# Kernel optimization log

Measured on AMD Instinct MI355X. Metric: run time of the kernel, lower is better.

The kernel has to match this reference:

```python
import jax, jax.numpy as jnp
import numpy as np

# Model dims (match init_kwargs)
E, D, H, K = 8, 512, 1024, 2   # num_experts, input/output dim, hidden dim, top_k
B, S = 4, 2048                 # batch, seq_len


def setup_inputs() -> dict:
    key = jax.random.key(0)
    ks = jax.random.split(key, 5)
    sd = lambda fan: np.float32(1.0 / np.sqrt(fan))
    return {
        "x": jax.random.normal(ks[0], (B, S, D), jnp.float32),
        "gate_w": jax.random.normal(ks[1], (D, E), jnp.float32) * sd(D),
        "gate_b": jnp.zeros((E,), jnp.float32),
        "w1": jax.random.normal(ks[2], (E, D, H), jnp.float32) * sd(D),
        "b1": jnp.zeros((E, H), jnp.float32),
        "w2": jax.random.normal(ks[3], (E, H, D), jnp.float32) * sd(H),
        "b2": jnp.zeros((E, D), jnp.float32),
    }


def reference(x, gate_w, gate_b, w1, b1, w2, b2):
    # x: [B, S, D]
    Bb, Ss, Dd = x.shape
    xf = x.reshape(-1, Dd)                              # [N, D], N = B*S

    # Router: softmax over experts, top-k, renormalize selected weights
    logits = xf @ gate_w + gate_b                        # [N, E]
    probs = jax.nn.softmax(logits, axis=-1)              # [N, E]
    top_w, top_i = jax.lax.top_k(probs, K)               # [N, K]
    top_w = top_w / top_w.sum(axis=-1, keepdims=True)

    # Per-token combine weight for each expert (0 if not routed).
    onehot = jax.nn.one_hot(top_i, E, dtype=probs.dtype)  # [N, K, E]
    combine = jnp.einsum("nke,nk->ne", onehot, top_w)     # [N, E]

    # Expert MLPs. Dropout is inactive at inference (identity).
    # h: [E, N, H]; GELU exact (torch nn.GELU default uses erf)
    h = jax.nn.gelu(jnp.einsum("nd,edh->enh", xf, w1) + b1[:, None, :],
                    approximate=False)
    y = jnp.einsum("enh,ehd->end", h, w2) + b2[:, None, :]  # [E, N, D]

    # Weighted combine: tokens not routed to expert e have combine[:, e] == 0.
    out = jnp.einsum("end,ne->nd", y, combine).reshape(Bb, Ss, Dd)
    return out, probs.reshape(Bb, Ss, E)
```

## Files before the change

kernel.cpp:

```cpp
#include <hip/hip_runtime.h>
#include <stdint.h>

#define N_TOK 8192
#define DIM   512
#define HID   1024
#define NE    8
#define NSLOT 16384
#define MAXSLOT 17408

typedef __attribute__((ext_vector_type(8))) short short8;
typedef __attribute__((ext_vector_type(4))) float f32x4;

#define W1T_OFF  0ull
#define W2T_OFF  8388608ull
#define H_OFF    16777216ull
#define Y_OFF    52428800ull
#define XBF_OFF  52428800ull
#define TOPI_OFF 70254592ull
#define TOPW_OFF 70320128ull
#define SLOT_OFF 70385664ull
#define ROWS_OFF 70451200ull
#define RW_OFF   70520832ull
#define CNT_OFF  70590464ull

__device__ __forceinline__ unsigned int f2bfu(float f) {
  union { float f; unsigned int i; } v; v.f = f;
  unsigned int u = v.i;
  return (u + 0x7FFFu + ((u >> 16) & 1u)) >> 16;
}
__device__ __forceinline__ float bf2f(unsigned int u) {
  union { unsigned int i; float f; } v; v.i = (u & 0xFFFFu) << 16; return v.f;
}
__device__ __forceinline__ float gelu_f(float x) {
  float x2 = x * x;
  float u = x * (1.59576912f + 0.07135481f * x2);
  float ez = __expf(-u);
  return x * __builtin_amdgcn_rcpf(1.0f + ez);
}
__device__ __forceinline__ void async16(void* lds, const void* g) {
  __builtin_amdgcn_global_load_lds(
      (const __attribute__((address_space(1))) unsigned int*)g,
      (__attribute__((address_space(3))) unsigned int*)lds, 16, 0, 0);
}

__global__ __launch_bounds__(256) void k_prep(
    const float* __restrict__ w1, const float* __restrict__ w2,
    unsigned short* __restrict__ w1t, unsigned short* __restrict__ w2t,
    const float* __restrict__ x, const float* __restrict__ gw,
    const float* __restrict__ gb, float* __restrict__ probs_out,
    int2* __restrict__ topi, float2* __restrict__ topw,
    unsigned short* __restrict__ xbf) {
  __shared__ unsigned short tile[64][68];
  int tid = threadIdx.x;
  if (blockIdx.x < 2048) {
    int b = blockIdx.x;
    const float* src; unsigned short* dst; int R, C;
    if (b < 1024) { int e = b >> 7; int t = b & 127;
      src = w1 + (size_t)e * 524288; dst = w1t + (size_t)e * 524288; R = 512; C = 1024;
      int tr = t >> 4, tc = t & 15;
      src += (size_t)tr * 64 * C + tc * 64; dst += (size_t)tc * 64 * R + tr * 64;
    } else { b -= 1024; int e = b >> 7; int t = b & 127;
      src = w2 + (size_t)e * 524288; dst = w2t + (size_t)e * 524288; R = 1024; C = 512;
      int tr = t >> 3, tc = t & 7;
      src += (size_t)tr * 64 * C + tc * 64; dst += (size_t)tc * 64 * R + tr * 64;
    }
#pragma unroll
    for (int i = 0; i < 4; ++i) {
      int l = i * 256 + tid;
      int r = l >> 4, c4 = (l & 15) << 2;
      float4 v = *(const float4*)(src + (size_t)r * C + c4);
      tile[r][c4 + 0] = (unsigned short)f2bfu(v.x);
      tile[r][c4 + 1] = (unsigned short)f2bfu(v.y);
      tile[r][c4 + 2] = (unsigned short)f2bfu(v.z);
      tile[r][c4 + 3] = (unsigned short)f2bfu(v.w);
    }
    __syncthreads();
#pragma unroll
    for (int i = 0; i < 2; ++i) {
      int l = i * 256 + tid;
      int rr = l >> 3, c8 = (l & 7) << 3;
      ushort4 a, b2v;
      a.x = tile[c8 + 0][rr]; a.y = tile[c8 + 1][rr];
      a.z = tile[c8 + 2][rr]; a.w = tile[c8 + 3][rr];
      b2v.x = tile[c8 + 4][rr]; b2v.y = tile[c8 + 5][rr];
      b2v.z = tile[c8 + 6][rr]; b2v.w = tile[c8 + 7][rr];
      uint4 pk;
      pk.x = (unsigned int)a.x | ((unsigned int)a.y << 16);
      pk.y = (unsigned int)a.z | ((unsigned int)a.w << 16);
      pk.z = (unsigned int)b2v.x | ((unsigned int)b2v.y << 16);
      pk.w = (unsigned int)b2v.z | ((unsigned int)b2v.w << 16);
      *(uint4*)(dst + (size_t)rr * R + c8) = pk;
    }
  } else {
    int wave = tid >> 6, lane = tid & 63;
    int n = (blockIdx.x - 2048) * 4 + wave;
    const float4* xr = (const float4*)(x + (size_t)n * DIM);
    float4 x0 = xr[lane * 2], x1 = xr[lane * 2 + 1];
    float xf[8] = {x0.x, x0.y, x0.z, x0.w, x1.x, x1.y, x1.z, x1.w};
    uint4 pa;
    pa.x = f2bfu(xf[0]) | (f2bfu(xf[1]) << 16);
    pa.y = f2bfu(xf[2]) | (f2bfu(xf[3]) << 16);
    pa.z = f2bfu(xf[4]) | (f2bfu(xf[5]) << 16);
    pa.w = f2bfu(xf[6]) | (f2bfu(xf[7]) << 16);
    *(uint4*)(xbf + (size_t)n * DIM + lane * 8) = pa;
    float acc[8] = {0.f,0.f,0.f,0.f,0.f,0.f,0.f,0.f};
    const float4* gwr = (const float4*)gw;
#pragma unroll
    for (int j = 0; j < 8; ++j) {
      int d = lane * 8 + j;
      float4 g0 = gwr[d * 2], g1 = gwr[d * 2 + 1];
      acc[0] += xf[j] * g0.x; acc[1] += xf[j] * g0.y; acc[2] += xf[j] * g0.z; acc[3] += xf[j] * g0.w;
      acc[4] += xf[j] * g1.x; acc[5] += xf[j] * g1.y; acc[6] += xf[j] * g1.z; acc[7] += xf[j] * g1.w;
    }
#pragma unroll
    for (int o = 1; o < 64; o <<= 1)
#pragma unroll
      for (int e = 0; e < 8; ++e) acc[e] += __shfl_xor(acc[e], o, 64);
    float p[8], mx = -1e30f, s = 0.f;
#pragma unroll
    for (int e = 0; e < 8; ++e) { p[e] = acc[e] + gb[e]; mx = fmaxf(mx, p[e]); }
#pragma unroll
    for (int e = 0; e < 8; ++e) { p[e] = __expf(p[e] - mx); s += p[e]; }
    float inv = 1.f / s;
#pragma unroll
    for (int e = 0; e < 8; ++e) p[e] *= inv;
    if (lane < 8) probs_out[(size_t)n * NE + lane] = p[lane];
    if (lane == 0) {
      int i0 = 0; float v0 = p[0];
#pragma unroll
      for (int e = 1; e < 8; ++e) if (p[e] > v0) { v0 = p[e]; i0 = e; }
      int i1 = -1; float v1 = -1.f;
#pragma unroll
      for (int e = 0; e < 8; ++e) if (e != i0 && p[e] > v1) { v1 = p[e]; i1 = e; }
      float sw = 1.f / (v0 + v1);
      topi[n] = make_int2(i0, i1);
      topw[n] = make_float2(v0 * sw, v1 * sw);
    }
  }
}

__global__ __launch_bounds__(1024) void k_countassign(
    const int2* __restrict__ topi, const float2* __restrict__ topw,
    int* __restrict__ meta, int* __restrict__ rows, float* __restrict__ rw,
    int* __restrict__ slot_of) {
  __shared__ int ch[32][8];
  __shared__ int tot[8], poff_s[9], tiles_s[8];
  __shared__ int sm_off[1024 * 8];
  int t = threadIdx.x, g = t >> 5;
  if (t < 256) ((int*)ch)[t] = 0;
  __syncthreads();
  int2 te[8]; float2 tw[8];
  int c[8] = {0,0,0,0,0,0,0,0};
  int base_tok = t * 8;
#pragma unroll
  for (int i = 0; i < 8; ++i) {
    te[i] = topi[base_tok + i];
    tw[i] = topw[base_tok + i];
#pragma unroll
    for (int k = 0; k < 8; ++k) c[k] += (te[i].x == k) + (te[i].y == k);
  }
#pragma unroll
  for (int k = 0; k < 8; ++k) if (c[k]) atomicAdd(&ch[g][k], c[k]);
#pragma unroll
  for (int k = 0; k < 8; ++k) {
    int s = c[k];
#pragma unroll
    for (int d = 1; d < 32; d <<= 1) {
      int u = __shfl_up(s, d, 32);
      if ((t & 31) >= d) s += u;
    }
    sm_off[t * 8 + k] = s - c[k];
  }
  __syncthreads();
  if (t < 8) {
    int a = 0;
#pragma unroll
    for (int b = 0; b < 32; ++b) { int v = ch[b][t]; ch[b][t] = a; a += v; }
    tot[t] = a; meta[t] = a;
  }
  __syncthreads();
  if (t == 0) {
    int a = 0, ts = 0;
#pragma unroll
    for (int e = 0; e < 8; ++e) {
      int tiles = (tot[e] + 127) >> 7;
      poff_s[e] = a; tiles_s[e] = tiles;
      meta[16 + e] = a; meta[32 + e] = ts;
      a += tiles << 7; ts += tiles;
    }
    poff_s[8] = a; meta[24] = a; meta[40] = ts;
  }
  __syncthreads();
#pragma unroll
  for (int i = 0; i < 8; ++i) {
    int n = base_tok + i;
    int e0 = te[i].x, e1 = te[i].y;
    int o0 = sm_off[t * 8 + e0]++;
    int s0 = poff_s[e0] + ch[g][e0] + o0;
    int o1 = sm_off[t * 8 + e1]++;
    int s1 = poff_s[e1] + ch[g][e1] + o1;
    rows[s0] = n; rw[s0] = tw[i].x; slot_of[2 * n] = s0;
    rows[s1] = n; rw[s1] = tw[i].y; slot_of[2 * n + 1] = s1;
  }
#pragma unroll
  for (int e = 0; e < 8; ++e) {
    int padn = (tiles_s[e] << 7) - tot[e];
    if (t < padn) {
      int s = poff_s[e] + tot[e] + t;
      rows[s] = 0; rw[s] = 0.f;
    }
  }
}

__global__ __launch_bounds__(256) void k_gemm1(
    const unsigned short* __restrict__ xbf, const unsigned short* __restrict__ w1t,
    const float* __restrict__ b1, const int* __restrict__ meta,
    const int* __restrict__ rows, unsigned short* __restrict__ h) {
  int lin = blockIdx.x;
  int xcd = lin & 7, j = lin >> 3;
  int t = xcd * 17 + (j >> 3);
  int nt = j & 7;
  if (t >= meta[40]) return;
  int e = 0;
#pragma unroll
  for (int i = 1; i < 8; ++i) if (t >= meta[32 + i]) e = i;
  int mt = t - meta[32 + e];
  int row0 = meta[16 + e] + (mt << 7);
  __shared__ __align__(16) unsigned short As[2][4096];
  __shared__ __align__(16) unsigned short Bs[2][4096];
  int tid = threadIdx.x;
  int wave = tid >> 6, lane = tid & 63;
  int wr = wave & 1, wc = wave >> 1;
  f32x4 acc[4][4] = {};
  const unsigned short* bBase = w1t + (size_t)e * HID * DIM + (size_t)(nt * 128) * DIM;

  const unsigned short* ga[2]; const unsigned short* gb[2];
#pragma unroll
  for (int jj = 0; jj < 2; ++jj) {
    int s = jj * 256 + tid;
    int r = s >> 2;
    int cg = ((s & 3) ^ ((r >> 1) & 3)) << 3;
    ga[jj] = xbf + (size_t)rows[row0 + r] * DIM + cg;
    gb[jj] = bBase + (size_t)r * DIM + cg;
  }
  int ldst = (wave * 64) * 8;

#pragma unroll
  for (int jj = 0; jj < 2; ++jj) {
    async16(&As[0][jj * 2048 + ldst], ga[jj]);
    async16(&Bs[0][jj * 2048 + ldst], gb[jj]);
  }
  __syncthreads();

  for (int k0 = 0; k0 < DIM; k0 += 32) {
    int cur = (k0 >> 5) & 1, nxt = cur ^ 1;
    if (k0 + 32 < DIM) {
#pragma unroll
      for (int jj = 0; jj < 2; ++jj) {
        async16(&As[nxt][jj * 2048 + ldst], ga[jj] + k0 + 32);
        async16(&Bs[nxt][jj * 2048 + ldst], gb[jj] + k0 + 32);
      }
    }
    {
      int ca = lane >> 4;
      short8 tf[4], wf[4];
#pragma unroll
      for (int am = 0; am < 4; ++am) {
        int ra = wr * 64 + am * 16 + (lane & 15);
        tf[am] = *(const short8*)&As[cur][(ra * 4 + (ca ^ ((ra >> 1) & 3))) * 8];
      }
#pragma unroll
      for (int an = 0; an < 4; ++an) {
        int rb = wc * 64 + an * 16 + (lane & 15);
        wf[an] = *(const short8*)&Bs[cur][(rb * 4 + (ca ^ ((rb >> 1) & 3))) * 8];
      }
#pragma unroll
      for (int an = 0; an < 4; ++an)
#pragma unroll
        for (int am = 0; am < 4; ++am)
          acc[an][am] = __builtin_amdgcn_mfma_f32_16x16x32_bf16(wf[an], tf[am], acc[an][am], 0, 0, 0);
    }
    __syncthreads();
  }
  int ml = lane & 15, q = lane >> 4;
#pragma unroll
  for (int am = 0; am < 4; ++am) {
    int slot_r = row0 + wr * 64 + am * 16 + ml;
    unsigned short* hrow = h + (size_t)slot_r * HID;
#pragma unroll
    for (int an = 0; an < 4; ++an) {
      int colb = nt * 128 + wc * 64 + an * 16 + q * 4;
      float4 bias = *(const float4*)&b1[e * HID + colb];
      f32x4 v = acc[an][am];
      float g0 = gelu_f(v[0] + bias.x);
      float g1 = gelu_f(v[1] + bias.y);
      float g2 = gelu_f(v[2] + bias.z);
      float g3 = gelu_f(v[3] + bias.w);
      uint2 pk;
      pk.x = f2bfu(g0) | (f2bfu(g1) << 16);
      pk.y = f2bfu(g2) | (f2bfu(g3) << 16);
      *(uint2*)(hrow + colb) = pk;
    }
  }
}

__global__ __launch_bounds__(256) void k_gemm2(
    const unsigned short* __restrict__ h, const unsigned short* __restrict__ w2t,
    const float* __restrict__ b2, const int* __restrict__ meta,
    const float* __restrict__ rw, unsigned short* __restrict__ y) {
  int lin = blockIdx.x;
  int xcd = lin & 7, j = lin >> 3;
  int t = xcd * 17 + (j >> 2);
  int nt = j & 3;
  if (t >= meta[40]) return;
  int e = 0;
#pragma unroll
  for (int i = 1; i < 8; ++i) if (t >= meta[32 + i]) e = i;
  int mt = t - meta[32 + e];
  int row0 = meta[16 + e] + (mt << 7);
  __shared__ __align__(16) unsigned short As[2][4096];
  __shared__ __align__(16) unsigned short Bs[2][4096];
  int tid = threadIdx.x;
  int wave = tid >> 6, lane = tid & 63;
  int wr = wave & 1, wc = wave >> 1;
  f32x4 acc[4][4] = {};
  const unsigned short* aBase = h + (size_t)row0 * HID;
  const unsigned short* bBase = w2t + (size_t)e * DIM * HID + (size_t)(nt * 128) * HID;

  const unsigned short* ga[2]; const unsigned short* gb[2];
#pragma unroll
  for (int jj = 0; jj < 2; ++jj) {
    int s = jj * 256 + tid;
    int r = s >> 2;
    int cg = ((s & 3) ^ ((r >> 1) & 3)) << 3;
    ga[jj] = aBase + (size_t)r * HID + cg;
    gb[jj] = bBase + (size_t)r * HID + cg;
  }
  int ldst = (wave * 64) * 8;

#pragma unroll
  for (int jj = 0; jj < 2; ++jj) {
    async16(&As[0][jj * 2048 + ldst], ga[jj]);
    async16(&Bs[0][jj * 2048 + ldst], gb[jj]);
  }
  __syncthreads();

  for (int k0 = 0; k0 < HID; k0 += 32) {
    int cur = (k0 >> 5) & 1, nxt = cur ^ 1;
    if (k0 + 32 < HID) {
#pragma unroll
      for (int jj = 0; jj < 2; ++jj) {
        async16(&As[nxt][jj * 2048 + ldst], ga[jj] + k0 + 32);
        async16(&Bs[nxt][jj * 2048 + ldst], gb[jj] + k0 + 32);
      }
    }
    {
      int ca = lane >> 4;
      short8 tf[4], wf[4];
#pragma unroll
      for (int am = 0; am < 4; ++am) {
        int ra = wr * 64 + am * 16 + (lane & 15);
        tf[am] = *(const short8*)&As[cur][(ra * 4 + (ca ^ ((ra >> 1) & 3))) * 8];
      }
#pragma unroll
      for (int an = 0; an < 4; ++an) {
        int rb = wc * 64 + an * 16 + (lane & 15);
        wf[an] = *(const short8*)&Bs[cur][(rb * 4 + (ca ^ ((rb >> 1) & 3))) * 8];
      }
#pragma unroll
      for (int an = 0; an < 4; ++an)
#pragma unroll
        for (int am = 0; am < 4; ++am)
          acc[an][am] = __builtin_amdgcn_mfma_f32_16x16x32_bf16(wf[an], tf[am], acc[an][am], 0, 0, 0);
    }
    __syncthreads();
  }
  int ml = lane & 15, q = lane >> 4;
#pragma unroll
  for (int am = 0; am < 4; ++am) {
    int slot_r = row0 + wr * 64 + am * 16 + ml;
    float w = rw[slot_r];
    unsigned short* yrow = y + (size_t)slot_r * DIM;
#pragma unroll
    for (int an = 0; an < 4; ++an) {
      int colb = nt * 128 + wc * 64 + an * 16 + q * 4;
      float4 bias = *(const float4*)&b2[e * DIM + colb];
      f32x4 v = acc[an][am];
      uint2 pk;
      pk.x = f2bfu((v[0] + bias.x) * w) | (f2bfu((v[1] + bias.y) * w) << 16);
      pk.y = f2bfu((v[2] + bias.z) * w) | (f2bfu((v[3] + bias.w) * w) << 16);
      *(uint2*)(yrow + colb) = pk;
    }
  }
}

__global__ __launch_bounds__(256) void k_combine(
    const unsigned short* __restrict__ y, const int* __restrict__ slot_of,
    float* __restrict__ out) {
  int t = blockIdx.x * 256 + threadIdx.x;
  int n = t >> 6, c = (t & 63) << 3;
  int s0 = slot_of[2 * n], s1 = slot_of[2 * n + 1];
  uint4 u0 = *(const uint4*)(y + (size_t)s0 * DIM + c);
  uint4 u1 = *(const uint4*)(y + (size_t)s1 * DIM + c);
  float4 o0, o1;
  o0.x = bf2f(u0.x) + bf2f(u1.x); o0.y = bf2f(u0.x >> 16) + bf2f(u1.x >> 16);
  o0.z = bf2f(u0.y) + bf2f(u1.y); o0.w = bf2f(u0.y >> 16) + bf2f(u1.y >> 16);
  o1.x = bf2f(u0.z) + bf2f(u1.z); o1.y = bf2f(u0.z >> 16) + bf2f(u1.z >> 16);
  o1.z = bf2f(u0.w) + bf2f(u1.w); o1.w = bf2f(u0.w >> 16) + bf2f(u1.w >> 16);
  *(float4*)(out + (size_t)n * DIM + c) = o0;
  *(float4*)(out + (size_t)n * DIM + c + 4) = o1;
}

extern "C" void kernel_launch(void* const* d_in, const int* in_sizes, int n_in,
                              void* d_out, int out_size, void* d_ws, size_t ws_size,
                              hipStream_t stream) {
  const float* x  = (const float*)d_in[0];
  const float* gw = (const float*)d_in[1];
  const float* gb = (const float*)d_in[2];
  const float* w1 = (const float*)d_in[3];
  const float* b1 = (const float*)d_in[4];
  const float* w2 = (const float*)d_in[5];
  const float* b2 = (const float*)d_in[6];
  float* out = (float*)d_out;
  char* ws = (char*)d_ws;

  unsigned short* w1t = (unsigned short*)(ws + W1T_OFF);
  unsigned short* w2t = (unsigned short*)(ws + W2T_OFF);
  unsigned short* h   = (unsigned short*)(ws + H_OFF);
  unsigned short* y   = (unsigned short*)(ws + Y_OFF);
  unsigned short* xbf = (unsigned short*)(ws + XBF_OFF);
  int2*   topi    = (int2*)(ws + TOPI_OFF);
  float2* topw    = (float2*)(ws + TOPW_OFF);
  int*    slot_of = (int*)(ws + SLOT_OFF);
  int*    rows    = (int*)(ws + ROWS_OFF);
  float*  rw      = (float*)(ws + RW_OFF);
  int*    meta    = (int*)(ws + CNT_OFF);
  float*  probs   = out + (size_t)N_TOK * DIM;

  k_prep       <<<dim3(4096), dim3(256),  0, stream>>>(w1, w2, w1t, w2t,
                                                       x, gw, gb, probs, topi, topw, xbf);
  k_countassign<<<dim3(1),    dim3(1024), 0, stream>>>(topi, topw, meta, rows, rw, slot_of);
  k_gemm1      <<<dim3(1088), dim3(256),  0, stream>>>(xbf, w1t, b1, meta, rows, h);
  k_gemm2      <<<dim3(544),  dim3(256),  0, stream>>>(h, w2t, b2, meta, rw, y);
  k_combine    <<<dim3(2048), dim3(256),  0, stream>>>(y, slot_of, out);
}
```

Baseline: 207.2 us.

## Load expert weight fragments directly from global, stage only activations in larger LDS chunks

Both expert GEMM kernels stop staging the weight (B) tile in shared memory. Each lane now reads its MFMA weight fragments straight from global memory. The activation (A) tile is staged in bigger 128-wide K chunks, double-buffered across 64 KB of LDS, so there are fewer barriers per K loop. This removes the LDS traffic and barriers for weights but makes MFMA issue wait on global/L2 latency for uncoalesced per-lane 16-byte weight loads. The larger LDS footprint may also reduce occupancy.

```diff
diff --git a/kernel.cpp b/kernel.cpp
--- a/kernel.cpp
+++ b/kernel.cpp
@@ -226,54 +226,52 @@
   for (int i = 1; i < 8; ++i) if (t >= meta[32 + i]) e = i;
   int mt = t - meta[32 + e];
   int row0 = meta[16 + e] + (mt << 7);
-  __shared__ __align__(16) unsigned short As[2][4096];
-  __shared__ __align__(16) unsigned short Bs[2][4096];
+  __shared__ __align__(16) unsigned short As[2][16384];
   int tid = threadIdx.x;
   int wave = tid >> 6, lane = tid & 63;
   int wr = wave & 1, wc = wave >> 1;
+  int ml = lane & 15, q = lane >> 4;
   f32x4 acc[4][4] = {};
   const unsigned short* bBase = w1t + (size_t)e * HID * DIM + (size_t)(nt * 128) * DIM;
 
-  const unsigned short* ga[2]; const unsigned short* gb[2];
-#pragma unroll
-  for (int jj = 0; jj < 2; ++jj) {
+  const unsigned short* wB[4];
+#pragma unroll
+  for (int an = 0; an < 4; ++an)
+    wB[an] = bBase + (size_t)(wc * 64 + an * 16 + ml) * DIM + q * 8;
+
+  const unsigned short* ga[8];
+#pragma unroll
+  for (int jj = 0; jj < 8; ++jj) {
     int s = jj * 256 + tid;
-    int r = s >> 2;
-    int cg = ((s & 3) ^ ((r >> 1) & 3)) << 3;
-    ga[jj] = xbf + (size_t)rows[row0 + r] * DIM + cg;
-    gb[jj] = bBase + (size_t)r * DIM + cg;
-  }
-  int ldst = (wave * 64) * 8;
-
-#pragma unroll
-  for (int jj = 0; jj < 2; ++jj) {
-    async16(&As[0][jj * 2048 + ldst], ga[jj]);
-    async16(&Bs[0][jj * 2048 + ldst], gb[jj]);
-  }
-  __syncthreads();
-
-  for (int k0 = 0; k0 < DIM; k0 += 32) {
-    int cur = (k0 >> 5) & 1, nxt = cur ^ 1;
-    if (k0 + 32 < DIM) {
-#pragma unroll
-      for (int jj = 0; jj < 2; ++jj) {
-        async16(&As[nxt][jj * 2048 + ldst], ga[jj] + k0 + 32);
-        async16(&Bs[nxt][jj * 2048 + ldst], gb[jj] + k0 + 32);
+    int ks = s >> 9, r = (s >> 2) & 127, c2 = s & 3;
+    int col = ks * 32 + ((c2 ^ ((r >> 1) & 3)) << 3);
+    ga[jj] = xbf + (size_t)rows[row0 + r] * DIM + col;
+  }
+
+#define STAGE1(buf, c) do { \
+    _Pragma("unroll") \
+    for (int jj = 0; jj < 8; ++jj) \
+      async16(&As[buf][(jj * 256 + wave * 64) * 8], ga[jj] + (c) * 128); \
+  } while (0)
+
+  STAGE1(0, 0);
+  __syncthreads();
+
+  for (int c = 0; c < 4; ++c) {
+    int cur = c & 1, nxt = cur ^ 1;
+    if (c < 3) STAGE1(nxt, c + 1);
+#pragma unroll
+    for (int ks = 0; ks < 4; ++ks) {
+      int kt = c * 4 + ks;
+      short8 tf[4], wf[4];
+#pragma unroll
+      for (int am = 0; am < 4; ++am) {
+        int ra = wr * 64 + am * 16 + ml;
+        tf[am] = *(const short8*)&As[cur][ks * 4096 + ra * 32 + ((q ^ ((ra >> 1) & 3)) << 3)];
       }
-    }
-    {
-      int ca = lane >> 4;
-      short8 tf[4], wf[4];
-#pragma unroll
-      for (int am = 0; am < 4; ++am) {
-        int ra = wr * 64 + am * 16 + (lane & 15);
-        tf[am] = *(const short8*)&As[cur][(ra * 4 + (ca ^ ((ra >> 1) & 3))) * 8];
-      }
-#pragma unroll
-      for (int an = 0; an < 4; ++an) {
-        int rb = wc * 64 + an * 16 + (lane & 15);
-        wf[an] = *(const short8*)&Bs[cur][(rb * 4 + (ca ^ ((rb >> 1) & 3))) * 8];
-      }
+#pragma unroll
+      for (int an = 0; an < 4; ++an)
+        wf[an] = *(const short8*)(wB[an] + kt * 32);
 #pragma unroll
       for (int an = 0; an < 4; ++an)
 #pragma unroll
@@ -282,7 +280,8 @@
     }
     __syncthreads();
   }
-  int ml = lane & 15, q = lane >> 4;
+#undef STAGE1
+
 #pragma unroll
   for (int am = 0; am < 4; ++am) {
     int slot_r = row0 + wr * 64 + am * 16 + ml;
@@ -318,55 +317,53 @@
   for (int i = 1; i < 8; ++i) if (t >= meta[32 + i]) e = i;
   int mt = t - meta[32 + e];
   int row0 = meta[16 + e] + (mt << 7);
-  __shared__ __align__(16) unsigned short As[2][4096];
-  __shared__ __align__(16) unsigned short Bs[2][4096];
+  __shared__ __align__(16) unsigned short As[2][16384];
   int tid = threadIdx.x;
   int wave = tid >> 6, lane = tid & 63;
   int wr = wave & 1, wc = wave >> 1;
+  int ml = lane & 15, q = lane >> 4;
   f32x4 acc[4][4] = {};
   const unsigned short* aBase = h + (size_t)row0 * HID;
   const unsigned short* bBase = w2t + (size_t)e * DIM * HID + (size_t)(nt * 128) * HID;
 
-  const unsigned short* ga[2]; const unsigned short* gb[2];
-#pragma unroll
-  for (int jj = 0; jj < 2; ++jj) {
+  const unsigned short* wB[4];
+#pragma unroll
+  for (int an = 0; an < 4; ++an)
+    wB[an] = bBase + (size_t)(wc * 64 + an * 16 + ml) * HID + q * 8;
+
+  const unsigned short* ga[8];
+#pragma unroll
+  for (int jj = 0; jj < 8; ++jj) {
     int s = jj * 256 + tid;
-    int r = s >> 2;
-    int cg = ((s & 3) ^ ((r >> 1) & 3)) << 3;
-    ga[jj] = aBase + (size_t)r * HID + cg;
-    gb[jj] = bBase + (size_t)r * HID + cg;
-  }
-  int ldst = (wave * 64) * 8;
-
-#pragma unroll
-  for (int jj = 0; jj < 2; ++jj) {
-    async16(&As[0][jj * 2048 + ldst], ga[jj]);
-    async16(&Bs[0][jj * 2048 + ldst], gb[jj]);
-  }
-  __syncthreads();
-
-  for (int k0 = 0; k0 < HID; k0 += 32) {
-    int cur = (k0 >> 5) & 1, nxt = cur ^ 1;
-    if (k0 + 32 < HID) {
-#pragma unroll
-      for (int jj = 0; jj < 2; ++jj) {
-        async16(&As[nxt][jj * 2048 + ldst], ga[jj] + k0 + 32);
-        async16(&Bs[nxt][jj * 2048 + ldst], gb[jj] + k0 + 32);
+    int ks = s >> 9, r = (s >> 2) & 127, c2 = s & 3;
+    int col = ks * 32 + ((c2 ^ ((r >> 1) & 3)) << 3);
+    ga[jj] = aBase + (size_t)r * HID + col;
+  }
+
+#define STAGE2(buf, c) do { \
+    _Pragma("unroll") \
+    for (int jj = 0; jj < 8; ++jj) \
+      async16(&As[buf][(jj * 256 + wave * 64) * 8], ga[jj] + (c) * 128); \
+  } while (0)
+
+  STAGE2(0, 0);
+  __syncthreads();
+
+  for (int c = 0; c < 8; ++c) {
+    int cur = c & 1, nxt = cur ^ 1;
+    if (c < 7) STAGE2(nxt, c + 1);
+#pragma unroll
+    for (int ks = 0; ks < 4; ++ks) {
+      int kt = c * 4 + ks;
+      short8 tf[4], wf[4];
+#pragma unroll
+      for (int am = 0; am < 4; ++am) {
+        int ra = wr * 64 + am * 16 + ml;
+        tf[am] = *(const short8*)&As[cur][ks * 4096 + ra * 32 + ((q ^ ((ra >> 1) & 3)) << 3)];
       }
-    }
-    {
-      int ca = lane >> 4;
-      short8 tf[4], wf[4];
-#pragma unroll
-      for (int am = 0; am < 4; ++am) {
-        int ra = wr * 64 + am * 16 + (lane & 15);
-        tf[am] = *(const short8*)&As[cur][(ra * 4 + (ca ^ ((ra >> 1) & 3))) * 8];
-      }
-#pragma unroll
-      for (int an = 0; an < 4; ++an) {
-        int rb = wc * 64 + an * 16 + (lane & 15);
-        wf[an] = *(const short8*)&Bs[cur][(rb * 4 + (ca ^ ((rb >> 1) & 3))) * 8];
-      }
+#pragma unroll
+      for (int an = 0; an < 4; ++an)
+        wf[an] = *(const short8*)(wB[an] + kt * 32);
 #pragma unroll
       for (int an = 0; an < 4; ++an)
 #pragma unroll
@@ -375,15 +372,17 @@
     }
     __syncthreads();
   }
-  int ml = lane & 15, q = lane >> 4;
+#undef STAGE2
+
+  int mll = lane & 15, qq = lane >> 4;
 #pragma unroll
   for (int am = 0; am < 4; ++am) {
-    int slot_r = row0 + wr * 64 + am * 16 + ml;
+    int slot_r = row0 + wr * 64 + am * 16 + mll;
     float w = rw[slot_r];
     unsigned short* yrow = y + (size_t)slot_r * DIM;
 #pragma unroll
     for (int an = 0; an < 4; ++an) {
-      int colb = nt * 128 + wc * 64 + an * 16 + q * 4;
+      int colb = nt * 128 + wc * 64 + an * 16 + qq * 4;
       float4 bias = *(const float4*)&b2[e * DIM + colb];
       f32x4 v = acc[an][am];
       uint2 pk;
```

Result: slower. 266.0 us (+28.4%).
